# Kernel tuning notes

Measured on AMD Instinct MI355X. Metric: run time of the kernel, lower is better.

The kernel has to match this reference:

```python
import jax, jax.numpy as jnp
import numpy as np

N, H, E, C, V, K = 4096, 256, 128, 32, 64, 20


def setup_inputs() -> dict:
    key = jax.random.key(0)
    ks = jax.random.split(key, 16)
    f = lambda k, s: jax.random.normal(k, s, dtype=jnp.float32)
    return {
        "vec": f(ks[0], (N, H)),
        "inp": f(ks[1], (N, E)),
        "h_prev": f(ks[2], (N, H)),
        "c_prev": f(ks[3], (N, H)),
        "Wlin": f(ks[4], (C, V, H)) * 0.05,
        "blin": f(ks[5], (C, V)) * 0.05,
        "Wec": f(ks[6], (2, H)) * 0.05,
        "bec": f(ks[7], (2,)) * 0.05,
        "Wrel": f(ks[8], (5, H)) * 0.05,
        "brel": f(ks[9], (5,)) * 0.05,
        "W_ih": f(ks[10], (K, 4 * H, E)) * 0.05,
        "b_ih": f(ks[11], (K, 4 * H)) * 0.05,
        "W_hh": f(ks[12], (K, 4 * H, H)) * 0.05,
        "b_hh": f(ks[13], (K, 4 * H)) * 0.05,
        "category": jax.random.randint(ks[14], (N,), 0, C, dtype=jnp.int32),
        "cell_id": jax.random.randint(ks[15], (N,), 0, K, dtype=jnp.int32),
        "true_idx": jax.random.randint(jax.random.fold_in(key, 100), (N,), 0, V, dtype=jnp.int32),
        "ec_idx": jax.random.randint(jax.random.fold_in(key, 101), (N,), 0, 2, dtype=jnp.int32),
        "rel_idx": jax.random.randint(jax.random.fold_in(key, 102), (N,), 0, 5, dtype=jnp.int32),
    }


def _ce(logits, targets):
    # per-row cross entropy (same math as nn.CrossEntropyLoss per example)
    logp = jax.nn.log_softmax(logits, axis=-1)
    return -jnp.take_along_axis(logp, targets[:, None], axis=-1)[:, 0]


def reference(vec, inp, h_prev, c_prev, Wlin, blin, Wec, bec, Wrel, brel,
              W_ih, b_ih, W_hh, b_hh, category, cell_id, true_idx, ec_idx, rel_idx):
    # --- get_log_odds: per-category tiny linear head, selected by category ---
    logits_all = jnp.einsum('nh,cvh->ncv', vec, Wlin) + blin          # [N,C,V]
    logits = jnp.take_along_axis(logits_all, category[:, None, None].astype(jnp.int32), axis=1)[:, 0]  # [N,V]
    logits_ec = vec @ Wec.T + bec                                      # [N,2]
    logits_rel = vec @ Wrel.T + brel                                   # [N,5]

    # --- calculate_loss: CE over valid children + ec + rel ---
    losses = _ce(logits, true_idx) + _ce(logits_ec, ec_idx) + _ce(logits_rel, rel_idx)  # [N]

    # --- get_next: per-child-index LSTMCell, selected by cell_id ---
    gates_all = (jnp.einsum('ne,kge->nkg', inp, W_ih)
                 + jnp.einsum('nh,kgh->nkg', h_prev, W_hh)
                 + b_ih + b_hh)                                        # [N,K,4H]
    gates = jnp.take_along_axis(gates_all, cell_id[:, None, None].astype(jnp.int32), axis=1)[:, 0]  # [N,4H]
    i, f, g, o = jnp.split(gates, 4, axis=-1)                          # torch LSTMCell gate order i,f,g,o
    c_next = jax.nn.sigmoid(f) * c_prev + jax.nn.sigmoid(i) * jnp.tanh(g)
    h_next = jax.nn.sigmoid(o) * jnp.tanh(c_next)

    # pack: [N, 1 + 2H] = loss | h_next | c_next
    return jnp.concatenate([losses[:, None], h_next, c_next], axis=-1)
```

## Files before the change

kernel.cpp:

```cpp
#include <hip/hip_runtime.h>
#include <hip/hip_bf16.h>
#include <math.h>

#define Nn 4096
#define Hdim 256
#define Edim 128
#define Cdim 32
#define Vdim 64
#define Kdim 20
#define G4H 1024
#define OUTS 513

#define NB 8
#define LMAXL 96
#define MAXG (NB * LMAXL)
#define MAXT2 192
#define GRID (MAXG + MAXT2)

typedef short bf16x8 __attribute__((ext_vector_type(8)));
typedef float f32x4 __attribute__((ext_vector_type(4)));

__device__ __forceinline__ float sigmoidf_(float x) { return 1.0f / (1.0f + expf(-x)); }

__device__ __forceinline__ bf16x8 cvt8(float4 f0, float4 f1) {
    bf16x8 r;
    __hip_bfloat16 h;
    h = __float2bfloat16(f0.x); r[0] = *(short*)&h;
    h = __float2bfloat16(f0.y); r[1] = *(short*)&h;
    h = __float2bfloat16(f0.z); r[2] = *(short*)&h;
    h = __float2bfloat16(f0.w); r[3] = *(short*)&h;
    h = __float2bfloat16(f1.x); r[4] = *(short*)&h;
    h = __float2bfloat16(f1.y); r[5] = *(short*)&h;
    h = __float2bfloat16(f1.z); r[6] = *(short*)&h;
    h = __float2bfloat16(f1.w); r[7] = *(short*)&h;
    return r;
}

__device__ __forceinline__ void gl_lds16(const float* g, void* l) {
    __builtin_amdgcn_global_load_lds((const __attribute__((address_space(1))) void*)g,
                                     (__attribute__((address_space(3))) void*)l, 16, 0, 0);
}

__device__ __forceinline__ int swz(int r) { return ((r & 3) << 1) | ((r >> 2) & 1); }

__global__ __launch_bounds__(256, 4) void k_all(
    const float* __restrict__ vec, const float* __restrict__ inp,
    const float* __restrict__ h_prev, const float* __restrict__ c_prev,
    const float* __restrict__ Wlin, const float* __restrict__ blin,
    const float* __restrict__ Wec, const float* __restrict__ bec,
    const float* __restrict__ Wrel, const float* __restrict__ brel,
    const float* __restrict__ W_ih, const float* __restrict__ b_ih,
    const float* __restrict__ W_hh, const float* __restrict__ b_hh,
    const int* __restrict__ category, const int* __restrict__ cell_id,
    const int* __restrict__ true_idx, const int* __restrict__ ec_idx, const int* __restrict__ rel_idx,
    float* __restrict__ out)
{
    __shared__ __align__(16) char smem[40960];
    int* cntR = (int*)smem;
    int* cntF = (int*)(smem + 8192);
    int* wsum = (int*)(smem + 8320);
    int* rows_tmp = (int*)(smem + 8448);

    int t = threadIdx.x;
    int w = t >> 6, l = t & 63;
    int l15 = l & 15, quad = l >> 4;
    int lrow8 = l >> 3, lslot = l & 7;
    bool is_lstm = blockIdx.x < MAXG;
    const int* key = is_lstm ? cell_id : category;
    int nbins = is_lstm ? Kdim : Cdim;

    for (int i = t; i < nbins * 16; i += 256) cntR[i] = 0;
    __syncthreads();
    int4 kv0 = ((const int4*)key)[t * 4 + 0];
    int4 kv1 = ((const int4*)key)[t * 4 + 1];
    int4 kv2 = ((const int4*)key)[t * 4 + 2];
    int4 kv3 = ((const int4*)key)[t * 4 + 3];
    int ks[16] = { kv0.x, kv0.y, kv0.z, kv0.w, kv1.x, kv1.y, kv1.z, kv1.w,
                   kv2.x, kv2.y, kv2.z, kv2.w, kv3.x, kv3.y, kv3.z, kv3.w };
    int rep = t & 15;
    #pragma unroll
    for (int j = 0; j < 16; j++) atomicAdd(&cntR[ks[j] * 16 + rep], 1);
    __syncthreads();
    if (t < nbins) {
        int s2 = 0;
        #pragma unroll
        for (int r2 = 0; r2 < 16; r2++) s2 += cntR[t * 16 + r2];
        cntF[t] = s2;
    }
    __syncthreads();

    int myk, s_idx, hb0 = 0, rcount, wlen;
    if (is_lstm) {
        int b = blockIdx.x & 7, pos = blockIdx.x >> 3;
        int u = -1, sf = 0, acc = 0;
        for (int uu = b; uu < Kdim * 4; uu += NB) {
            int n = (cntF[uu >> 2] + 63) >> 6;
            if (u < 0 && pos < acc + n) { u = uu; sf = pos - acc; }
            acc += n;
        }
        if (u < 0) return;
        myk = u >> 2; hb0 = (u & 3) * 64; s_idx = sf;
        wlen = 64;
        rcount = min(64, cntF[myk] - s_idx * 64);
    } else {
        int slot = blockIdx.x - MAXG;
        int u = -1, sf = 0, acc = 0;
        for (int m = 0; m < Cdim; m++) {
            int n = (cntF[m] + 31) >> 5;
            if (u < 0 && slot < acc + n) { u = m; sf = slot - acc; }
            acc += n;
        }
        if (u < 0) return;
        myk = u; s_idx = sf;
        wlen = 32;
        rcount = min(32, cntF[myk] - s_idx * 32);
    }

    {
        int local = 0;
        #pragma unroll
        for (int j = 0; j < 16; j++) local += (ks[j] == myk) ? 1 : 0;
        int v = local;
        #pragma unroll
        for (int off = 1; off < 64; off <<= 1) {
            int n = __shfl_up(v, off);
            if (l >= off) v += n;
        }
        if (l == 63) wsum[w] = v;
        __syncthreads();
        int wbase = 0;
        #pragma unroll
        for (int ww = 0; ww < 4; ww++) wbase += (ww < w) ? wsum[ww] : 0;
        int rank = wbase + v - local;
        int w0 = s_idx * wlen;
        #pragma unroll
        for (int j = 0; j < 16; j++) {
            if (ks[j] == myk) {
                int rr = rank - w0;
                if (rr >= 0 && rr < wlen) rows_tmp[rr] = t * 16 + j;
                rank++;
            }
        }
        __syncthreads();
        if (t < wlen && t >= rcount) rows_tmp[t] = rows_tmp[0];
        __syncthreads();
    }
    int reg_row = rows_tmp[is_lstm ? l : (l & 31)];
    int swz_l = swz(l15);
    int p0 = (quad * 2) ^ swz_l;

    if (is_lstm) {
        float* Wbuf = (float*)smem;
        float* Xbuf = (float*)(smem + 32768);
        const float* Wih_k = W_ih + (size_t)myk * G4H * Edim;
        const float* Whh_k = W_hh + (size_t)myk * G4H * Hdim;

        int xr0 = w * 16 + lrow8;
        int xr1 = w * 16 + 8 + lrow8;
        int xrow0 = __shfl(reg_row, xr0);
        int xrow1 = __shfl(reg_row, xr1);
        int xg0 = lslot ^ swz(xr0);
        int xg1 = lslot ^ swz(xr1);

        f32x4 acc[4][4];
        #pragma unroll
        for (int m = 0; m < 4; m++)
            #pragma unroll
            for (int g = 0; g < 4; g++)
                acc[m][g] = (f32x4){0.f, 0.f, 0.f, 0.f};

        for (int st = 0; st < 12; st++) {
            int k0 = st * 32;
            const float* Wsrc; int stride, ko;
            if (k0 < Edim) { Wsrc = Wih_k; stride = Edim; ko = k0; }
            else           { Wsrc = Whh_k; stride = Hdim; ko = k0 - Edim; }
            const float* Xs0 = (k0 < Edim) ? inp + (size_t)xrow0 * Edim + ko
                                           : h_prev + (size_t)xrow0 * Hdim + (ko - 0);
            const float* Xs1 = (k0 < Edim) ? inp + (size_t)xrow1 * Edim + ko
                                           : h_prev + (size_t)xrow1 * Hdim + (ko - 0);
            __syncthreads();
            #pragma unroll
            for (int j = 0; j < 8; j++) {
                int r = w * 64 + j * 8 + lrow8;
                int g = lslot ^ swz(r);
                int gate = r >> 6, hl = r & 63;
                gl_lds16(Wsrc + (size_t)(gate * Hdim + hb0 + hl) * stride + ko + g * 4,
                         Wbuf + (w * 64 + j * 8) * 32);
            }
            gl_lds16(Xs0 + xg0 * 4, Xbuf + (w * 16) * 32);
            gl_lds16(Xs1 + xg1 * 4, Xbuf + (w * 16 + 8) * 32);
            __syncthreads();

            bf16x8 af[4], bfr[4];
            #pragma unroll
            for (int m = 0; m < 4; m++) {
                int row = m * 16 + l15;
                float4 lo = *(float4*)(Xbuf + row * 32 + p0 * 4);
                float4 hi = *(float4*)(Xbuf + row * 32 + (p0 ^ 1) * 4);
                af[m] = cvt8(lo, hi);
            }
            #pragma unroll
            for (int g = 0; g < 4; g++) {
                int row = g * 64 + w * 16 + l15;
                float4 lo = *(float4*)(Wbuf + row * 32 + p0 * 4);
                float4 hi = *(float4*)(Wbuf + row * 32 + (p0 ^ 1) * 4);
                bfr[g] = cvt8(lo, hi);
            }
            #pragma unroll
            for (int m = 0; m < 4; m++)
                #pragma unroll
                for (int g = 0; g < 4; g++)
                    acc[m][g] = __builtin_amdgcn_mfma_f32_16x16x32_bf16(af[m], bfr[g], acc[m][g], 0, 0, 0);
        }

        int h = hb0 + w * 16 + l15;
        float bs[4];
        #pragma unroll
        for (int g = 0; g < 4; g++)
            bs[g] = b_ih[(size_t)myk * G4H + g * Hdim + h] + b_hh[(size_t)myk * G4H + g * Hdim + h];

        #pragma unroll
        for (int m = 0; m < 4; m++) {
            #pragma unroll
            for (int reg = 0; reg < 4; reg++) {
                int r = m * 16 + quad * 4 + reg;
                int row = __shfl(reg_row, r);
                if (r < rcount) {
                    float iv = acc[m][0][reg] + bs[0];
                    float fv = acc[m][1][reg] + bs[1];
                    float gv = acc[m][2][reg] + bs[2];
                    float ov = acc[m][3][reg] + bs[3];
                    float cp = c_prev[(size_t)row * Hdim + h];
                    float cn = sigmoidf_(fv) * cp + sigmoidf_(iv) * tanhf(gv);
                    float hn = sigmoidf_(ov) * tanhf(cn);
                    out[(size_t)row * OUTS + 1 + h] = hn;
                    out[(size_t)row * OUTS + 1 + Hdim + h] = cn;
                }
            }
        }
    } else {
        float* Wlbuf = (float*)smem;
        float* Vbuf  = (float*)(smem + 10240);
        float* Lg    = (float*)(smem + 14336);
        int m2 = myk;

        int xr = w * 8 + lrow8;
        int xrow = __shfl(reg_row, xr);
        int xg = lslot ^ swz(xr);

        f32x4 a0[2], a1[2];
        #pragma unroll
        for (int m = 0; m < 2; m++) { a0[m] = (f32x4){0.f,0.f,0.f,0.f}; a1[m] = (f32x4){0.f,0.f,0.f,0.f}; }

        for (int st = 0; st < 8; st++) {
            int ko = st * 32;
            __syncthreads();
            for (int n = w; n < 10; n += 4) {
                int r = n * 8 + lrow8;
                int g = lslot ^ swz(r);
                const float* srcW;
                if (r < 64)      srcW = Wlin + ((size_t)m2 * Vdim + r) * Hdim;
                else if (r < 66) srcW = Wec + (size_t)(r - 64) * Hdim;
                else if (r < 71) srcW = Wrel + (size_t)(r - 66) * Hdim;
                else             srcW = Wlin + (size_t)m2 * Vdim * Hdim;
                gl_lds16(srcW + ko + g * 4, Wlbuf + n * 8 * 32);
            }
            gl_lds16(vec + (size_t)xrow * Hdim + ko + xg * 4, Vbuf + (w * 8) * 32);
            __syncthreads();

            bf16x8 af[2];
            #pragma unroll
            for (int m = 0; m < 2; m++) {
                int row = m * 16 + l15;
                float4 lo = *(float4*)(Vbuf + row * 32 + p0 * 4);
                float4 hi = *(float4*)(Vbuf + row * 32 + (p0 ^ 1) * 4);
                af[m] = cvt8(lo, hi);
            }
            {
                int row = w * 16 + l15;
                float4 lo = *(float4*)(Wlbuf + row * 32 + p0 * 4);
                float4 hi = *(float4*)(Wlbuf + row * 32 + (p0 ^ 1) * 4);
                bf16x8 b0 = cvt8(lo, hi);
                a0[0] = __builtin_amdgcn_mfma_f32_16x16x32_bf16(af[0], b0, a0[0], 0, 0, 0);
                a0[1] = __builtin_amdgcn_mfma_f32_16x16x32_bf16(af[1], b0, a0[1], 0, 0, 0);
            }
            if (w == 3) {
                int row = 64 + l15;
                float4 lo = *(float4*)(Wlbuf + row * 32 + p0 * 4);
                float4 hi = *(float4*)(Wlbuf + row * 32 + (p0 ^ 1) * 4);
                bf16x8 b1 = cvt8(lo, hi);
                a1[0] = __builtin_amdgcn_mfma_f32_16x16x32_bf16(af[0], b1, a1[0], 0, 0, 0);
                a1[1] = __builtin_amdgcn_mfma_f32_16x16x32_bf16(af[1], b1, a1[1], 0, 0, 0);
            }
        }
        __syncthreads();
        {
            int col = w * 16 + l15;
            float bb = blin[m2 * Vdim + col];
            #pragma unroll
            for (int m = 0; m < 2; m++)
                #pragma unroll
                for (int reg = 0; reg < 4; reg++)
                    Lg[(m * 16 + quad * 4 + reg) * 84 + col] = a0[m][reg] + bb;
            if (w == 3) {
                int col1 = 64 + l15;
                float bb1 = (l15 < 2) ? bec[l15] : ((l15 < 7) ? brel[l15 - 2] : 0.f);
                #pragma unroll
                for (int m = 0; m < 2; m++)
                    #pragma unroll
                    for (int reg = 0; reg < 4; reg++)
                        Lg[(m * 16 + quad * 4 + reg) * 84 + col1] = a1[m][reg] + bb1;
            }
        }
        __syncthreads();
        for (int rr = 0; rr < 8; rr++) {
            int r = w * 8 + rr;
            if (r >= rcount) break;
            int orig = __shfl(reg_row, r);
            float lg = Lg[r * 84 + l];
            float mx = lg;
            for (int ss = 32; ss >= 1; ss >>= 1) mx = fmaxf(mx, __shfl_xor(mx, ss));
            float sm = expf(lg - mx);
            for (int ss = 32; ss >= 1; ss >>= 1) sm += __shfl_xor(sm, ss);
            float lt = __shfl(lg, true_idx[orig]);
            float loss = mx + logf(sm) - lt;
            if (l == 0) {
                float l0 = Lg[r * 84 + 64], l1 = Lg[r * 84 + 65];
                float me2 = fmaxf(l0, l1);
                loss += me2 + logf(expf(l0 - me2) + expf(l1 - me2)) - ((ec_idx[orig] == 0) ? l0 : l1);
                float rl[5] = { Lg[r * 84 + 66], Lg[r * 84 + 67], Lg[r * 84 + 68], Lg[r * 84 + 69], Lg[r * 84 + 70] };
                float mr = rl[0];
                #pragma unroll
                for (int i = 1; i < 5; i++) mr = fmaxf(mr, rl[i]);
                float sr = 0.f;
                #pragma unroll
                for (int i = 0; i < 5; i++) sr += expf(rl[i] - mr);
                loss += mr + logf(sr) - rl[rel_idx[orig]];
                out[(size_t)orig * OUTS] = loss;
            }
        }
    }
}

extern "C" void kernel_launch(void* const* d_in, const int* in_sizes, int n_in,
                              void* d_out, int out_size, void* d_ws, size_t ws_size,
                              hipStream_t stream) {
    const float* vec      = (const float*)d_in[0];
    const float* inp      = (const float*)d_in[1];
    const float* h_prev   = (const float*)d_in[2];
    const float* c_prev   = (const float*)d_in[3];
    const float* Wlin     = (const float*)d_in[4];
    const float* blin     = (const float*)d_in[5];
    const float* Wec      = (const float*)d_in[6];
    const float* bec      = (const float*)d_in[7];
    const float* Wrel     = (const float*)d_in[8];
    const float* brel     = (const float*)d_in[9];
    const float* W_ih     = (const float*)d_in[10];
    const float* b_ih     = (const float*)d_in[11];
    const float* W_hh     = (const float*)d_in[12];
    const float* b_hh     = (const float*)d_in[13];
    const int*   category = (const int*)d_in[14];
    const int*   cell_id  = (const int*)d_in[15];
    const int*   true_idx = (const int*)d_in[16];
    const int*   ec_idx   = (const int*)d_in[17];
    const int*   rel_idx  = (const int*)d_in[18];
    float* out = (float*)d_out;

    k_all<<<GRID, 256, 0, stream>>>(
        vec, inp, h_prev, c_prev, Wlin, blin, Wec, bec, Wrel, brel,
        W_ih, b_ih, W_hh, b_hh, category, cell_id, true_idx, ec_idx, rel_idx, out);
}
```

Measured before the change: 154.0 us.

## Double-buffer LSTM weight staging and halve rows per block to 32

The LSTM gate GEMM now prefetches the next K-slice of weights and activations into a second LDS buffer with async global-to-LDS loads while computing on the current one, synchronised through manual vmcnt waits and raw barriers. The row tile per block drops from 64 to 32, which doubles the number of LSTM blocks (LMAXL raised) and halves the accumulators. LDS moves to a 72KB dynamic allocation, and the launch-bounds occupancy hint is removed. The smaller row tile means each weight slice is reloaded by twice as many blocks, so weight traffic goes up. The larger LDS footprint also lowers the number of blocks that can be resident per CU.

```diff
diff --git a/kernel.cpp b/kernel.cpp
--- a/kernel.cpp
+++ b/kernel.cpp
@@ -12,10 +12,11 @@
 #define OUTS 513
 
 #define NB 8
-#define LMAXL 96
+#define LMAXL 160
 #define MAXG (NB * LMAXL)
 #define MAXT2 192
 #define GRID (MAXG + MAXT2)
+#define DYN_LDS 73728
 
 typedef short bf16x8 __attribute__((ext_vector_type(8)));
 typedef float f32x4 __attribute__((ext_vector_type(4)));
@@ -43,7 +44,11 @@
 
 __device__ __forceinline__ int swz(int r) { return ((r & 3) << 1) | ((r >> 2) & 1); }
 
-__global__ __launch_bounds__(256, 4) void k_all(
+#define RBAR()   asm volatile("s_barrier" ::: "memory")
+#define WAITV9() asm volatile("s_waitcnt vmcnt(9)" ::: "memory")
+#define WAITV0() asm volatile("s_waitcnt vmcnt(0)" ::: "memory")
+
+__global__ __launch_bounds__(256) void k_all(
     const float* __restrict__ vec, const float* __restrict__ inp,
     const float* __restrict__ h_prev, const float* __restrict__ c_prev,
     const float* __restrict__ Wlin, const float* __restrict__ blin,
@@ -55,7 +60,7 @@
     const int* __restrict__ true_idx, const int* __restrict__ ec_idx, const int* __restrict__ rel_idx,
     float* __restrict__ out)
 {
-    __shared__ __align__(16) char smem[40960];
+    extern __shared__ __align__(16) char smem[];
     int* cntR = (int*)smem;
     int* cntF = (int*)(smem + 8192);
     int* wsum = (int*)(smem + 8320);
@@ -94,14 +99,14 @@
         int b = blockIdx.x & 7, pos = blockIdx.x >> 3;
         int u = -1, sf = 0, acc = 0;
         for (int uu = b; uu < Kdim * 4; uu += NB) {
-            int n = (cntF[uu >> 2] + 63) >> 6;
+            int n = (cntF[uu >> 2] + 31) >> 5;
             if (u < 0 && pos < acc + n) { u = uu; sf = pos - acc; }
             acc += n;
         }
         if (u < 0) return;
         myk = u >> 2; hb0 = (u & 3) * 64; s_idx = sf;
-        wlen = 64;
-        rcount = min(64, cntF[myk] - s_idx * 64);
+        wlen = 32;
+        rcount = min(32, cntF[myk] - s_idx * 32);
     } else {
         int slot = blockIdx.x - MAXG;
         int u = -1, sf = 0, acc = 0;
@@ -145,72 +150,76 @@
         if (t < wlen && t >= rcount) rows_tmp[t] = rows_tmp[0];
         __syncthreads();
     }
-    int reg_row = rows_tmp[is_lstm ? l : (l & 31)];
+    int reg_row = rows_tmp[l & 31];
     int swz_l = swz(l15);
     int p0 = (quad * 2) ^ swz_l;
 
     if (is_lstm) {
-        float* Wbuf = (float*)smem;
-        float* Xbuf = (float*)(smem + 32768);
         const float* Wih_k = W_ih + (size_t)myk * G4H * Edim;
         const float* Whh_k = W_hh + (size_t)myk * G4H * Hdim;
 
-        int xr0 = w * 16 + lrow8;
-        int xr1 = w * 16 + 8 + lrow8;
-        int xrow0 = __shfl(reg_row, xr0);
-        int xrow1 = __shfl(reg_row, xr1);
-        int xg0 = lslot ^ swz(xr0);
-        int xg1 = lslot ^ swz(xr1);
-
-        f32x4 acc[4][4];
-        #pragma unroll
-        for (int m = 0; m < 4; m++)
+        int xr = w * 8 + lrow8;
+        int xrow = __shfl(reg_row, xr);
+        int xg = lslot ^ swz(xr);
+
+        f32x4 acc[2][4];
+        #pragma unroll
+        for (int m = 0; m < 2; m++)
             #pragma unroll
             for (int g = 0; g < 4; g++)
                 acc[m][g] = (f32x4){0.f, 0.f, 0.f, 0.f};
 
-        for (int st = 0; st < 12; st++) {
+        auto stage = [&](int st, int sel) {
             int k0 = st * 32;
             const float* Wsrc; int stride, ko;
             if (k0 < Edim) { Wsrc = Wih_k; stride = Edim; ko = k0; }
             else           { Wsrc = Whh_k; stride = Hdim; ko = k0 - Edim; }
-            const float* Xs0 = (k0 < Edim) ? inp + (size_t)xrow0 * Edim + ko
-                                           : h_prev + (size_t)xrow0 * Hdim + (ko - 0);
-            const float* Xs1 = (k0 < Edim) ? inp + (size_t)xrow1 * Edim + ko
-                                           : h_prev + (size_t)xrow1 * Hdim + (ko - 0);
-            __syncthreads();
+            char* wb = smem + sel * 32768;
+            char* xb = smem + 65536 + sel * 4096;
             #pragma unroll
             for (int j = 0; j < 8; j++) {
                 int r = w * 64 + j * 8 + lrow8;
                 int g = lslot ^ swz(r);
                 int gate = r >> 6, hl = r & 63;
                 gl_lds16(Wsrc + (size_t)(gate * Hdim + hb0 + hl) * stride + ko + g * 4,
-                         Wbuf + (w * 64 + j * 8) * 32);
-            }
-            gl_lds16(Xs0 + xg0 * 4, Xbuf + (w * 16) * 32);
-            gl_lds16(Xs1 + xg1 * 4, Xbuf + (w * 16 + 8) * 32);
-            __syncthreads();
-
-            bf16x8 af[4], bfr[4];
-            #pragma unroll
-            for (int m = 0; m < 4; m++) {
-                int row = m * 16 + l15;
-                float4 lo = *(float4*)(Xbuf + row * 32 + p0 * 4);
-                float4 hi = *(float4*)(Xbuf + row * 32 + (p0 ^ 1) * 4);
-                af[m] = cvt8(lo, hi);
-            }
-            #pragma unroll
-            for (int g = 0; g < 4; g++) {
-                int row = g * 64 + w * 16 + l15;
-                float4 lo = *(float4*)(Wbuf + row * 32 + p0 * 4);
-                float4 hi = *(float4*)(Wbuf + row * 32 + (p0 ^ 1) * 4);
-                bfr[g] = cvt8(lo, hi);
-            }
-            #pragma unroll
-            for (int m = 0; m < 4; m++)
-                #pragma unroll
-                for (int g = 0; g < 4; g++)
-                    acc[m][g] = __builtin_amdgcn_mfma_f32_16x16x32_bf16(af[m], bfr[g], acc[m][g], 0, 0, 0);
+                         wb + (w * 64 + j * 8) * 128);
+            }
+            const float* xs = (k0 < Edim) ? inp + (size_t)xrow * Edim + ko
+                                          : h_prev + (size_t)xrow * Hdim + ko;
+            gl_lds16(xs + xg * 4, xb + (w * 8) * 128);
+        };
+
+        stage(0, 0);
+        for (int st = 0; st < 12; st++) {
+            int sel = st & 1;
+            if (st < 11) { stage(st + 1, sel ^ 1); WAITV9(); }
+            else         { WAITV0(); }
+            RBAR();
+            {
+                float* Wbuf = (float*)(smem + sel * 32768);
+                float* Xbuf = (float*)(smem + 65536 + sel * 4096);
+                bf16x8 af[2], bfr[4];
+                #pragma unroll
+                for (int m = 0; m < 2; m++) {
+                    int row = m * 16 + l15;
+                    float4 lo = *(float4*)(Xbuf + row * 32 + p0 * 4);
+                    float4 hi = *(float4*)(Xbuf + row * 32 + (p0 ^ 1) * 4);
+                    af[m] = cvt8(lo, hi);
+                }
+                #pragma unroll
+                for (int g = 0; g < 4; g++) {
+                    int row = g * 64 + w * 16 + l15;
+                    float4 lo = *(float4*)(Wbuf + row * 32 + p0 * 4);
+                    float4 hi = *(float4*)(Wbuf + row * 32 + (p0 ^ 1) * 4);
+                    bfr[g] = cvt8(lo, hi);
+                }
+                #pragma unroll
+                for (int m = 0; m < 2; m++)
+                    #pragma unroll
+                    for (int g = 0; g < 4; g++)
+                        acc[m][g] = __builtin_amdgcn_mfma_f32_16x16x32_bf16(af[m], bfr[g], acc[m][g], 0, 0, 0);
+            }
+            RBAR();
         }
 
         int h = hb0 + w * 16 + l15;
@@ -220,7 +229,7 @@
             bs[g] = b_ih[(size_t)myk * G4H + g * Hdim + h] + b_hh[(size_t)myk * G4H + g * Hdim + h];
 
         #pragma unroll
-        for (int m = 0; m < 4; m++) {
+        for (int m = 0; m < 2; m++) {
             #pragma unroll
             for (int reg = 0; reg < 4; reg++) {
                 int r = m * 16 + quad * 4 + reg;
@@ -366,7 +375,7 @@
     const int*   rel_idx  = (const int*)d_in[18];
     float* out = (float*)d_out;
 
-    k_all<<<GRID, 256, 0, stream>>>(
+    k_all<<<GRID, 256, DYN_LDS, stream>>>(
         vec, inp, h_prev, c_prev, Wlin, blin, Wec, bec, Wrel, brel,
         W_ih, b_ih, W_hh, b_hh, category, cell_id, true_idx, ec_idx, rel_idx, out);
 }
```

New measurement: 159.0 us. 1.03x slower.
